# Performance work log

Measured on AMD Instinct MI355X. Metric: run time of the kernel, lower is better.

Reference implementation:

```python
import jax, jax.numpy as jnp
import numpy as np

B, N, I = 8, 1024, 64
E, H, D = 2, 2, 128   # edge types, heads per layer, hidden dim
O = 64                # num_outputs
IN1 = E * H * D       # layer-1 filter input dim (concat of layer-0 heads)


def setup_inputs() -> dict:
    key = jax.random.key(0)
    ks = jax.random.split(key, 20)
    s = lambda f: 1.0 / np.sqrt(f)
    inp = {
        "nodes": jax.random.normal(ks[0], (B, N, I), jnp.float32),
        "edges": jax.random.normal(ks[1], (B, N, N, E), jnp.float32) * 0.1,
        "Wemb": jax.random.normal(ks[2], (I, D), jnp.float32) * s(I),
        "bemb": jnp.zeros((D,), jnp.float32),
        # layer 0 params: filter W, att nets a1/a2 (weight + bias), state bias
        "W0":   jax.random.normal(ks[3], (E, H, D, D), jnp.float32) * s(D),
        "A1w0": jax.random.normal(ks[4], (E, H, D), jnp.float32) * s(D),
        "A1b0": jnp.zeros((E, H), jnp.float32),
        "A2w0": jax.random.normal(ks[5], (E, H, D), jnp.float32) * s(D),
        "A2b0": jnp.zeros((E, H), jnp.float32),
        "SB0":  jnp.zeros((E, H, D), jnp.float32),
        # layer 1 params (input dim = E*H*D from concat)
        "W1":   jax.random.normal(ks[6], (E, H, IN1, D), jnp.float32) * s(IN1),
        "A1w1": jax.random.normal(ks[7], (E, H, D), jnp.float32) * s(D),
        "A1b1": jnp.zeros((E, H), jnp.float32),
        "A2w1": jax.random.normal(ks[8], (E, H, D), jnp.float32) * s(D),
        "A2b1": jnp.zeros((E, H), jnp.float32),
        "SB1":  jnp.zeros((E, H, D), jnp.float32),
        "Wout": jax.random.normal(ks[9], (D, O), jnp.float32) * s(D),
        "bout": jnp.zeros((O,), jnp.float32),
    }
    return inp


def _gat_layer(state, edges_ebnn, W, a1w, a1b, a2w, a2b, sb):
    # state: (B,N,Fin); W: (E,H,Fin,D); edges_ebnn: (E,1,B,N,N)
    Wh = jnp.einsum('bni,ehid->ehbnd', state, W)                    # (E,H,B,N,D)
    s1 = jnp.einsum('ehbnd,ehd->ehbn', Wh, a1w) + a1b[:, :, None, None]
    s2 = jnp.einsum('ehbnd,ehd->ehbn', Wh, a2w) + a2b[:, :, None, None]
    att = s1[..., :, None] + s2[..., None, :]                       # a1_i + a2_j
    att = jax.nn.leaky_relu(att, 0.2) + edges_ebnn                  # edge-type bias
    att = jax.nn.softmax(att, axis=-2)                              # torch dim=1 (over i)
    msg = jnp.einsum('ehbij,ehbjd->ehbid', att, Wh)                 # bmm aggregation
    return msg + sb[:, :, None, None, :]                            # (E,H,B,N,D)


def reference(nodes, edges, Wemb, bemb,
              W0, A1w0, A1b0, A2w0, A2b0, SB0,
              W1, A1w1, A1b1, A2w1, A2b1, SB1,
              Wout, bout):
    edges_e = jnp.transpose(edges, (3, 0, 1, 2))[:, None]           # (E,1,B,N,N)
    state = jax.nn.relu(nodes @ Wemb + bemb)                        # SlimFC embedding
    # layer 0: concat heads/edgetypes along feature dim (torch order jj outer, ii inner)
    m0 = _gat_layer(state, edges_e, W0, A1w0, A1b0, A2w0, A2b0, SB0)
    state = jnp.transpose(m0, (2, 3, 0, 1, 4)).reshape(B, N, E * H * D)
    # layer 1 (last): elu then mean over all heads/edgetypes
    m1 = jax.nn.elu(_gat_layer(state, edges_e, W1, A1w1, A1b1, A2w1, A2b1, SB1))
    state = jnp.mean(m1, axis=(0, 1))                               # (B,N,D)
    return state @ Wout + bout                                      # (B,N,O)
```

## Files before the change

### kernel.cpp

```cpp
#include <hip/hip_runtime.h>
#include <hip/hip_bf16.h>
#include <math.h>

#define NB 8
#define NN 1024
#define NI 64
#define EHC 4
#define ND 128
#define NO 64
#define FIN1 512
#define BN 8192

typedef __attribute__((ext_vector_type(8))) short short8;
typedef __attribute__((ext_vector_type(4))) float f32x4;

__device__ __forceinline__ unsigned short f2bf(float f) {
    union { float f; unsigned u; } v; v.f = f;
    unsigned r = v.u + 0x7FFF + ((v.u >> 16) & 1);
    return (unsigned short)(r >> 16);
}

__global__ void prepTk(const float* __restrict__ W0, const float* __restrict__ W1,
                       const float* __restrict__ Wemb, unsigned short* __restrict__ W0T,
                       unsigned short* __restrict__ W1T, unsigned short* __restrict__ WembT) {
    int idx = blockIdx.x * 256 + threadIdx.x;
    if (idx < EHC * ND * ND) {
        int eh = idx >> 14, d = (idx >> 7) & 127, k = idx & 127;
        W0T[idx] = f2bf(W0[((size_t)(eh * ND + k)) * ND + d]);
    }
    int idx1 = idx - EHC * ND * ND;
    if (idx1 >= 0 && idx1 < EHC * ND * FIN1) {
        int eh = idx1 >> 16;
        int r = idx1 & 65535;
        int d = r >> 9, k = r & 511;
        W1T[idx1] = f2bf(W1[((size_t)(eh * FIN1 + k)) * ND + d]);
    }
    int idx2 = idx - (EHC * ND * ND + EHC * ND * FIN1);
    if (idx2 >= 0 && idx2 < ND * NI) {
        int d = idx2 >> 6, k = idx2 & 63;
        WembT[idx2] = f2bf(Wemb[k * ND + d]);
    }
}

__global__ __launch_bounds__(256, 4) void embwh0k(
    const float* __restrict__ nodes, const unsigned short* __restrict__ WembT,
    const float* __restrict__ bemb, const unsigned short* __restrict__ W0T,
    unsigned short* __restrict__ WhT, const float* __restrict__ a1w,
    const float* __restrict__ a1b, const float* __restrict__ a2w,
    const float* __restrict__ a2b, float* __restrict__ s1, float* __restrict__ s2) {
    int id = blockIdx.x;
    int g = id & 7, s_ = id >> 3;
    int eh = s_ & 3;
    int row0 = ((s_ >> 2) * 8 + g) * 32;
    int t = threadIdx.x;
    int w = t >> 6, lane = t & 63;
    int m = lane & 15, quad = lane >> 4;

    __shared__ unsigned short stateL[32 * 136];

    f32x4 accE[2][2];
#pragma unroll
    for (int mt = 0; mt < 2; ++mt)
#pragma unroll
        for (int nt = 0; nt < 2; ++nt) accE[mt][nt] = (f32x4){0.f, 0.f, 0.f, 0.f};
#pragma unroll
    for (int kt = 0; kt < 2; ++kt) {
        short8 aE[2], bE[2];
#pragma unroll
        for (int mt = 0; mt < 2; ++mt) {
            const float* np = nodes + (size_t)(row0 + mt * 16 + m) * NI + kt * 32 + quad * 8;
            f32x4 v0 = *(const f32x4*)np;
            f32x4 v1 = *(const f32x4*)(np + 4);
            union { unsigned short us[8]; short8 s8; } pk;
#pragma unroll
            for (int r = 0; r < 4; ++r) {
                pk.us[r] = f2bf(v0[r]);
                pk.us[r + 4] = f2bf(v1[r]);
            }
            aE[mt] = pk.s8;
        }
#pragma unroll
        for (int nt = 0; nt < 2; ++nt)
            bE[nt] = *(const short8*)(WembT + (w * 32 + nt * 16 + m) * NI + kt * 32 + quad * 8);
#pragma unroll
        for (int mt = 0; mt < 2; ++mt)
#pragma unroll
            for (int nt = 0; nt < 2; ++nt)
                accE[mt][nt] =
                    __builtin_amdgcn_mfma_f32_16x16x32_bf16(aE[mt], bE[nt], accE[mt][nt], 0, 0, 0);
    }
#pragma unroll
    for (int mt = 0; mt < 2; ++mt)
#pragma unroll
        for (int nt = 0; nt < 2; ++nt) {
            int d = w * 32 + nt * 16 + m;
            float bb = bemb[d];
#pragma unroll
            for (int r = 0; r < 4; ++r) {
                float v = fmaxf(accE[mt][nt][r] + bb, 0.f);
                stateL[(mt * 16 + quad * 4 + r) * 136 + d] = f2bf(v);
            }
        }
    __syncthreads();

    f32x4 acc[2][2];
#pragma unroll
    for (int mt = 0; mt < 2; ++mt)
#pragma unroll
        for (int nt = 0; nt < 2; ++nt) acc[mt][nt] = (f32x4){0.f, 0.f, 0.f, 0.f};
#pragma unroll
    for (int k0 = 0; k0 < ND; k0 += 32) {
        short8 a[2], b[2];
#pragma unroll
        for (int mt = 0; mt < 2; ++mt)
            a[mt] = *(const short8*)&stateL[(mt * 16 + m) * 136 + k0 + quad * 8];
#pragma unroll
        for (int nt = 0; nt < 2; ++nt)
            b[nt] = *(const short8*)(W0T + ((size_t)(eh * ND + w * 32 + nt * 16 + m)) * ND +
                                     k0 + quad * 8);
#pragma unroll
        for (int mt = 0; mt < 2; ++mt)
#pragma unroll
            for (int nt = 0; nt < 2; ++nt)
                acc[mt][nt] =
                    __builtin_amdgcn_mfma_f32_16x16x32_bf16(a[mt], b[nt], acc[mt][nt], 0, 0, 0);
    }

    int b_ = row0 >> 10, i0b = row0 & 1023;
    int ehb = eh * NB + b_;
#pragma unroll
    for (int mt = 0; mt < 2; ++mt)
#pragma unroll
        for (int nt = 0; nt < 2; ++nt) {
            int d = w * 32 + nt * 16 + m;
            int i = i0b + mt * 16 + quad * 4;
            union { unsigned short us[4]; unsigned long long u64; } pk;
#pragma unroll
            for (int r = 0; r < 4; ++r) pk.us[r] = f2bf(acc[mt][nt][r]);
            *(unsigned long long*)(WhT + (((size_t)ehb) * ND + d) * NN + i) = pk.u64;
        }
    float w1a = a1w[eh * ND + w * 32 + m], w1b = a1w[eh * ND + w * 32 + 16 + m];
    float w2a = a2w[eh * ND + w * 32 + m], w2b = a2w[eh * ND + w * 32 + 16 + m];
    float p1[2][4], p2[2][4];
#pragma unroll
    for (int mt = 0; mt < 2; ++mt)
#pragma unroll
        for (int r = 0; r < 4; ++r) {
            p1[mt][r] = acc[mt][0][r] * w1a + acc[mt][1][r] * w1b;
            p2[mt][r] = acc[mt][0][r] * w2a + acc[mt][1][r] * w2b;
        }
#pragma unroll
    for (int off = 8; off >= 1; off >>= 1)
#pragma unroll
        for (int mt = 0; mt < 2; ++mt)
#pragma unroll
            for (int r = 0; r < 4; ++r) {
                p1[mt][r] += __shfl_xor(p1[mt][r], off);
                p2[mt][r] += __shfl_xor(p2[mt][r], off);
            }
    __shared__ float sred[2][4][4][8];
    if (m == 0) {
#pragma unroll
        for (int mt = 0; mt < 2; ++mt)
#pragma unroll
            for (int r = 0; r < 4; ++r) {
                sred[0][w][quad][mt * 4 + r] = p1[mt][r];
                sred[1][w][quad][mt * 4 + r] = p2[mt][r];
            }
    }
    __syncthreads();
    if (t < 32) {
        int mt = t >> 4, quad2 = (t >> 2) & 3, r = t & 3;
        int c = mt * 4 + r;
        float v = sred[0][0][quad2][c] + sred[0][1][quad2][c] + sred[0][2][quad2][c] +
                  sred[0][3][quad2][c];
        s1[(size_t)ehb * NN + i0b + t] = v + a1b[eh];
    } else if (t < 64) {
        int tl = t - 32;
        int mt = tl >> 4, quad2 = (tl >> 2) & 3, r = tl & 3;
        int c = mt * 4 + r;
        float v = sred[1][0][quad2][c] + sred[1][1][quad2][c] + sred[1][2][quad2][c] +
                  sred[1][3][quad2][c];
        s2[(size_t)ehb * NN + i0b + tl] = v + a2b[eh];
    }
}

__global__ __launch_bounds__(256, 4) void whgemm1k(
    const unsigned short* __restrict__ state, const unsigned short* __restrict__ WT,
    unsigned short* __restrict__ WhT, const float* __restrict__ a1w,
    const float* __restrict__ a1b, const float* __restrict__ a2w,
    const float* __restrict__ a2b, float* __restrict__ s1, float* __restrict__ s2) {
    int id = blockIdx.x;
    int g = id & 7, s_ = id >> 3;
    int eh = s_ & 3;
    int row0 = ((s_ >> 2) * 8 + g) * 32;
    int t = threadIdx.x;
    int w = t >> 6, lane = t & 63;
    int m = lane & 15, quad = lane >> 4;

    f32x4 acc[2][2];
#pragma unroll
    for (int mt = 0; mt < 2; ++mt)
#pragma unroll
        for (int nt = 0; nt < 2; ++nt) acc[mt][nt] = (f32x4){0.f, 0.f, 0.f, 0.f};

    const unsigned short* Ab = state + (size_t)(row0 + m) * FIN1 + quad * 8;
    const unsigned short* Bb = WT + ((size_t)eh * ND + w * 32 + m) * FIN1 + quad * 8;
#pragma unroll 4
    for (int k0 = 0; k0 < FIN1; k0 += 32) {
        short8 a[2], b[2];
#pragma unroll
        for (int mt = 0; mt < 2; ++mt)
            a[mt] = *(const short8*)(Ab + (size_t)mt * 16 * FIN1 + k0);
#pragma unroll
        for (int nt = 0; nt < 2; ++nt)
            b[nt] = *(const short8*)(Bb + (size_t)nt * 16 * FIN1 + k0);
#pragma unroll
        for (int mt = 0; mt < 2; ++mt)
#pragma unroll
            for (int nt = 0; nt < 2; ++nt)
                acc[mt][nt] =
                    __builtin_amdgcn_mfma_f32_16x16x32_bf16(a[mt], b[nt], acc[mt][nt], 0, 0, 0);
    }
    int b_ = row0 >> 10, i0b = row0 & 1023;
    int ehb = eh * NB + b_;
#pragma unroll
    for (int mt = 0; mt < 2; ++mt)
#pragma unroll
        for (int nt = 0; nt < 2; ++nt) {
            int d = w * 32 + nt * 16 + m;
            int i = i0b + mt * 16 + quad * 4;
            union { unsigned short us[4]; unsigned long long u64; } pk;
#pragma unroll
            for (int r = 0; r < 4; ++r) pk.us[r] = f2bf(acc[mt][nt][r]);
            *(unsigned long long*)(WhT + (((size_t)ehb) * ND + d) * NN + i) = pk.u64;
        }
    float w1a = a1w[eh * ND + w * 32 + m], w1b = a1w[eh * ND + w * 32 + 16 + m];
    float w2a = a2w[eh * ND + w * 32 + m], w2b = a2w[eh * ND + w * 32 + 16 + m];
    float p1[2][4], p2[2][4];
#pragma unroll
    for (int mt = 0; mt < 2; ++mt)
#pragma unroll
        for (int r = 0; r < 4; ++r) {
            p1[mt][r] = acc[mt][0][r] * w1a + acc[mt][1][r] * w1b;
            p2[mt][r] = acc[mt][0][r] * w2a + acc[mt][1][r] * w2b;
        }
#pragma unroll
    for (int off = 8; off >= 1; off >>= 1)
#pragma unroll
        for (int mt = 0; mt < 2; ++mt)
#pragma unroll
            for (int r = 0; r < 4; ++r) {
                p1[mt][r] += __shfl_xor(p1[mt][r], off);
                p2[mt][r] += __shfl_xor(p2[mt][r], off);
            }
    __shared__ float sred[2][4][4][8];
    if (m == 0) {
#pragma unroll
        for (int mt = 0; mt < 2; ++mt)
#pragma unroll
            for (int r = 0; r < 4; ++r) {
                sred[0][w][quad][mt * 4 + r] = p1[mt][r];
                sred[1][w][quad][mt * 4 + r] = p2[mt][r];
            }
    }
    __syncthreads();
    if (t < 32) {
        int mt = t >> 4, quad2 = (t >> 2) & 3, r = t & 3;
        int c = mt * 4 + r;
        float v = sred[0][0][quad2][c] + sred[0][1][quad2][c] + sred[0][2][quad2][c] +
                  sred[0][3][quad2][c];
        s1[(size_t)ehb * NN + i0b + t] = v + a1b[eh];
    } else if (t < 64) {
        int tl = t - 32;
        int mt = tl >> 4, quad2 = (tl >> 2) & 3, r = tl & 3;
        int c = mt * 4 + r;
        float v = sred[1][0][quad2][c] + sred[1][1][quad2][c] + sred[1][2][quad2][c] +
                  sred[1][3][quad2][c];
        s2[(size_t)ehb * NN + i0b + tl] = v + a2b[eh];
    }
}

__global__ __launch_bounds__(256, 4) void colsumk(const float* __restrict__ edges,
                                                  const float* __restrict__ s1,
                                                  const float* __restrict__ s2,
                                                  float* __restrict__ Spart) {
    int jt = blockIdx.x, b = blockIdx.y, ic = blockIdx.z;
    int t = threadIdx.x;
    int jl = t & 63, is = t >> 6;
    int j = jt * 64 + jl;
    __shared__ float s1L[4][128];
    for (int idx = t; idx < 512; idx += 256) {
        int eh = idx >> 7;
        s1L[eh][idx & 127] = s1[((size_t)eh * NB + b) * NN + ic * 128 + (idx & 127)];
    }
    __syncthreads();
    float s2v[4], acc4[4];
#pragma unroll
    for (int eh = 0; eh < 4; ++eh) {
        s2v[eh] = s2[((size_t)eh * NB + b) * NN + j];
        acc4[eh] = 0.f;
    }
    const float2* ep = (const float2*)edges + ((size_t)(b * NN + ic * 128 + is * 32)) * NN + j;
#pragma unroll 8
    for (int ii = 0; ii < 32; ++ii) {
        float2 ev = ep[(size_t)ii * NN];
        int il = is * 32 + ii;
#pragma unroll
        for (int eh = 0; eh < 4; ++eh) {
            float x = s1L[eh][il] + s2v[eh];
            x = x >= 0.f ? x : 0.2f * x;
            float a = x + (eh < 2 ? ev.x : ev.y);
            acc4[eh] += __expf(a);
        }
    }
    __shared__ float red[4][4][64];
#pragma unroll
    for (int eh = 0; eh < 4; ++eh) red[is][eh][jl] = acc4[eh];
    __syncthreads();
    if (t < 256) {
        int eho = t >> 6, jlo = t & 63;
        float Sv = red[0][eho][jlo] + red[1][eho][jlo] + red[2][eho][jlo] + red[3][eho][jlo];
        Spart[(((size_t)ic * EHC + eho) * NB + b) * NN + jt * 64 + jlo] = Sv;
    }
}

__global__ __launch_bounds__(256, 4) void msgk(const float* __restrict__ edges,
                                               const unsigned short* __restrict__ WhT,
                                               const float* __restrict__ s1,
                                               const float* __restrict__ s2,
                                               const float* __restrict__ Spart,
                                               const float* __restrict__ sb,
                                               unsigned short* __restrict__ out0,
                                               float* __restrict__ out1, int mode) {
    int id = blockIdx.x;
    int b = id & 7;
    int s_ = id >> 3;
    int eh = s_ & 3;
    int itile = s_ >> 2;
    int e = eh >> 1;
    int i0 = itile * 64;
    int t = threadIdx.x;
    int w = t >> 6, lane = t & 63;
    int n = lane & 15, quad = lane >> 4;
    int jl = t & 63, ib = w;

    __shared__ float2 stL[NN];
    __shared__ unsigned short pA[2][64 * 72];

    int base = (eh * NB + b) * NN;
    const size_t pstr = (size_t)EHC * NB * NN;
    for (int jj = t; jj < NN; jj += 256) {
        float S = 0.f;
#pragma unroll
        for (int ic = 0; ic < 8; ++ic) S += Spart[(size_t)ic * pstr + base + jj];
        stL[jj] = make_float2(s2[base + jj], __logf(S));
    }
    float s1r[16];
    {
        const f32x4* sp = (const f32x4*)(s1 + base + i0 + ib * 16);
#pragma unroll
        for (int q4 = 0; q4 < 4; ++q4) {
            f32x4 v = sp[q4];
#pragma unroll
            for (int r = 0; r < 4; ++r) s1r[q4 * 4 + r] = v[r];
        }
    }

    f32x4 acc[2][4];
#pragma unroll
    for (int mt = 0; mt < 2; ++mt)
#pragma unroll
        for (int nt = 0; nt < 4; ++nt) acc[mt][nt] = (f32x4){0.f, 0.f, 0.f, 0.f};

    const unsigned short* Ab =
        WhT + ((size_t)base * ND + (size_t)(w * 32 + n) * NN) + quad * 8;
    const float2* ep = (const float2*)edges + (size_t)(b * NN + i0 + ib * 16) * NN + jl;
    __syncthreads();

    for (int st16 = 0; st16 < 16; ++st16) {
        int j0 = st16 * 64;
        int buf = st16 & 1;
        float2 stj = stL[j0 + jl];
#pragma unroll
        for (int q = 0; q < 16; ++q) {
            float2 ev = ep[(size_t)q * NN + j0];
            float edge = e ? ev.y : ev.x;
            float x = s1r[q] + stj.x;
            x = x >= 0.f ? x : 0.2f * x;
            pA[buf][(ib * 16 + q) * 72 + jl] = f2bf(__expf(x + edge - stj.y));
        }
        __syncthreads();
#pragma unroll
        for (int kt = 0; kt < 2; ++kt) {
            short8 av[2], bv[4];
#pragma unroll
            for (int mt = 0; mt < 2; ++mt)
                av[mt] = *(const short8*)(Ab + (size_t)mt * 16 * NN + kt * 32 + j0);
#pragma unroll
            for (int nt = 0; nt < 4; ++nt)
                bv[nt] = *(const short8*)&pA[buf][(nt * 16 + n) * 72 + kt * 32 + quad * 8];
#pragma unroll
            for (int mt = 0; mt < 2; ++mt)
#pragma unroll
                for (int nt = 0; nt < 4; ++nt)
                    acc[mt][nt] = __builtin_amdgcn_mfma_f32_16x16x32_bf16(av[mt], bv[nt],
                                                                          acc[mt][nt], 0, 0, 0);
        }
    }

#pragma unroll
    for (int mt = 0; mt < 2; ++mt) {
        int d0 = w * 32 + mt * 16 + quad * 4;
        f32x4 sbv = *(const f32x4*)&sb[eh * ND + d0];
#pragma unroll
        for (int nt = 0; nt < 4; ++nt) {
            int i = i0 + nt * 16 + n;
            if (mode == 0) {
                union { unsigned short us[4]; unsigned long long u64; } pk;
#pragma unroll
                for (int r = 0; r < 4; ++r) pk.us[r] = f2bf(acc[mt][nt][r] + sbv[r]);
                *(unsigned long long*)(out0 + (size_t)(b * NN + i) * FIN1 + eh * ND + d0) =
                    pk.u64;
            } else {
                f32x4 vv;
#pragma unroll
                for (int r = 0; r < 4; ++r) {
                    float v = acc[mt][nt][r] + sbv[r];
                    vv[r] = v > 0.f ? v : expm1f(v);
                }
                *(f32x4*)(out1 + ((size_t)(eh * NB + b) * NN + i) * ND + d0) = vv;
            }
        }
    }
}

__global__ __launch_bounds__(256) void finalk(const float* __restrict__ m1,
                                              const float* __restrict__ Wout,
                                              const float* __restrict__ bout,
                                              float* __restrict__ out) {
    int row0 = blockIdx.x * 16;
    int t = threadIdx.x;
    __shared__ float sF[16 * ND];
    __shared__ float wL[ND * NO];
    const size_t str = (size_t)BN * ND;
    for (int idx = t; idx < 16 * ND; idx += 256) {
        size_t r = (size_t)row0 * ND + idx;
        sF[idx] = 0.25f * (m1[r] + m1[r + str] + m1[r + 2 * str] + m1[r + 3 * str]);
    }
    for (int idx = t; idx < ND * NO; idx += 256) wL[idx] = Wout[idx];
    __syncthreads();
    int o = t & 63;
    int rr = t >> 6;
    float bo = bout[o];
#pragma unroll
    for (int q = 0; q < 4; ++q) {
        int r = rr * 4 + q;
        float acc = 0.f;
#pragma unroll 4
        for (int d = 0; d < ND; ++d) acc += sF[r * ND + d] * wL[d * NO + o];
        out[(size_t)(row0 + r) * NO + o] = acc + bo;
    }
}

extern "C" void kernel_launch(void* const* d_in, const int* in_sizes, int n_in,
                              void* d_out, int out_size, void* d_ws, size_t ws_size,
                              hipStream_t stream) {
    const float* nodes = (const float*)d_in[0];
    const float* edges = (const float*)d_in[1];
    const float* Wemb = (const float*)d_in[2];
    const float* bemb = (const float*)d_in[3];
    const float* W0 = (const float*)d_in[4];
    const float* A1w0 = (const float*)d_in[5];
    const float* A1b0 = (const float*)d_in[6];
    const float* A2w0 = (const float*)d_in[7];
    const float* A2b0 = (const float*)d_in[8];
    const float* SB0 = (const float*)d_in[9];
    const float* W1 = (const float*)d_in[10];
    const float* A1w1 = (const float*)d_in[11];
    const float* A1b1 = (const float*)d_in[12];
    const float* A2w1 = (const float*)d_in[13];
    const float* A2b1 = (const float*)d_in[14];
    const float* SB1 = (const float*)d_in[15];
    const float* Wout = (const float*)d_in[16];
    const float* bout = (const float*)d_in[17];
    float* out = (float*)d_out;

    char* p = (char*)d_ws;
    auto alloc = [&](size_t bytes) {
        char* r = p;
        p += (bytes + 255) & ~(size_t)255;
        return r;
    };
    unsigned short* W0T = (unsigned short*)alloc((size_t)EHC * ND * ND * 2);
    unsigned short* W1T = (unsigned short*)alloc((size_t)EHC * ND * FIN1 * 2);
    unsigned short* WembT = (unsigned short*)alloc((size_t)ND * NI * 2);
    unsigned short* WhT = (unsigned short*)alloc((size_t)EHC * BN * ND * 2);
    unsigned short* state1 = (unsigned short*)alloc((size_t)BN * FIN1 * 2);
    float* s1b = (float*)alloc((size_t)EHC * BN * 4);
    float* s2b = (float*)alloc((size_t)EHC * BN * 4);
    float* Spart = (float*)alloc((size_t)8 * EHC * BN * 4);
    float* m1 = (float*)alloc((size_t)EHC * BN * ND * 4);

    prepTk<<<1312, 256, 0, stream>>>(W0, W1, Wemb, W0T, W1T, WembT);
    embwh0k<<<1024, 256, 0, stream>>>(nodes, WembT, bemb, W0T, WhT, A1w0, A1b0, A2w0, A2b0,
                                      s1b, s2b);
    colsumk<<<dim3(NN / 64, NB, 8), 256, 0, stream>>>(edges, s1b, s2b, Spart);
    msgk<<<512, 256, 0, stream>>>(edges, WhT, s1b, s2b, Spart, SB0, state1, m1, 0);
    whgemm1k<<<1024, 256, 0, stream>>>(state1, W1T, WhT, A1w1, A1b1, A2w1, A2b1, s1b, s2b);
    colsumk<<<dim3(NN / 64, NB, 8), 256, 0, stream>>>(edges, s1b, s2b, Spart);
    msgk<<<512, 256, 0, stream>>>(edges, WhT, s1b, s2b, Spart, SB1, state1, m1, 1);
    finalk<<<BN / 16, 256, 0, stream>>>(m1, Wout, bout, out);
}
```

Before: 285.4 us.

## Double-buffer msg kernel loads with 512-thread blocks and vectorize colsum edge reads

The message kernel now runs 512 threads per block. Each wave owns 16 output rows and computes 8 softmax rows, and the edge values and Wh fragments for the next j-tile are prefetched into registers while the current tile runs (software pipelining). Colsum reads edges as float4, covering two j columns per thread, and reduces over 8 partial slices. The aim is to hide global load latency and raise memory throughput. The cost is more registers per thread and more threads per block, which may limit occupancy under launch_bounds(512,4).

```diff
diff --git a/kernel.cpp b/kernel.cpp
--- a/kernel.cpp
+++ b/kernel.cpp
@@ -287,45 +287,57 @@
                                                   float* __restrict__ Spart) {
     int jt = blockIdx.x, b = blockIdx.y, ic = blockIdx.z;
     int t = threadIdx.x;
-    int jl = t & 63, is = t >> 6;
-    int j = jt * 64 + jl;
+    int jp = t & 31, is = t >> 5;
+    int j = jt * 64 + jp * 2;
     __shared__ float s1L[4][128];
     for (int idx = t; idx < 512; idx += 256) {
         int eh = idx >> 7;
         s1L[eh][idx & 127] = s1[((size_t)eh * NB + b) * NN + ic * 128 + (idx & 127)];
     }
     __syncthreads();
-    float s2v[4], acc4[4];
+    float s2v[4][2], acc4[4][2];
 #pragma unroll
     for (int eh = 0; eh < 4; ++eh) {
-        s2v[eh] = s2[((size_t)eh * NB + b) * NN + j];
-        acc4[eh] = 0.f;
-    }
-    const float2* ep = (const float2*)edges + ((size_t)(b * NN + ic * 128 + is * 32)) * NN + j;
-#pragma unroll 8
-    for (int ii = 0; ii < 32; ++ii) {
-        float2 ev = ep[(size_t)ii * NN];
-        int il = is * 32 + ii;
+        s2v[eh][0] = s2[((size_t)eh * NB + b) * NN + j];
+        s2v[eh][1] = s2[((size_t)eh * NB + b) * NN + j + 1];
+        acc4[eh][0] = 0.f;
+        acc4[eh][1] = 0.f;
+    }
+    const float4* ep = (const float4*)edges +
+                       (size_t)(b * NN + ic * 128 + is * 16) * (NN / 2) + jt * 32 + jp;
+#pragma unroll 4
+    for (int ii = 0; ii < 16; ++ii) {
+        float4 ev = ep[(size_t)ii * (NN / 2)];
+        float s1v = s1L[0][is * 16 + ii];
 #pragma unroll
         for (int eh = 0; eh < 4; ++eh) {
-            float x = s1L[eh][il] + s2v[eh];
-            x = x >= 0.f ? x : 0.2f * x;
-            float a = x + (eh < 2 ? ev.x : ev.y);
-            acc4[eh] += __expf(a);
-        }
-    }
-    __shared__ float red[4][4][64];
-#pragma unroll
-    for (int eh = 0; eh < 4; ++eh) red[is][eh][jl] = acc4[eh];
+            float sv = s1L[eh][is * 16 + ii];
+            float x0 = sv + s2v[eh][0];
+            x0 = fmaxf(x0, 0.2f * x0);
+            acc4[eh][0] += __expf(x0 + (eh < 2 ? ev.x : ev.y));
+            float x1 = sv + s2v[eh][1];
+            x1 = fmaxf(x1, 0.2f * x1);
+            acc4[eh][1] += __expf(x1 + (eh < 2 ? ev.z : ev.w));
+        }
+        (void)s1v;
+    }
+    __shared__ float red[8][4][64];
+#pragma unroll
+    for (int eh = 0; eh < 4; ++eh) {
+        red[is][eh][jp * 2] = acc4[eh][0];
+        red[is][eh][jp * 2 + 1] = acc4[eh][1];
+    }
     __syncthreads();
     if (t < 256) {
         int eho = t >> 6, jlo = t & 63;
-        float Sv = red[0][eho][jlo] + red[1][eho][jlo] + red[2][eho][jlo] + red[3][eho][jlo];
+        float Sv = 0.f;
+#pragma unroll
+        for (int isx = 0; isx < 8; ++isx) Sv += red[isx][eho][jlo];
         Spart[(((size_t)ic * EHC + eho) * NB + b) * NN + jt * 64 + jlo] = Sv;
     }
 }
 
-__global__ __launch_bounds__(256, 4) void msgk(const float* __restrict__ edges,
+__global__ __launch_bounds__(512, 4) void msgk(const float* __restrict__ edges,
                                                const unsigned short* __restrict__ WhT,
                                                const float* __restrict__ s1,
                                                const float* __restrict__ s2,
@@ -350,68 +362,80 @@
 
     int base = (eh * NB + b) * NN;
     const size_t pstr = (size_t)EHC * NB * NN;
-    for (int jj = t; jj < NN; jj += 256) {
+    for (int jj = t; jj < NN; jj += 512) {
         float S = 0.f;
 #pragma unroll
         for (int ic = 0; ic < 8; ++ic) S += Spart[(size_t)ic * pstr + base + jj];
         stL[jj] = make_float2(s2[base + jj], __logf(S));
     }
-    float s1r[16];
+    float s1r[8];
     {
-        const f32x4* sp = (const f32x4*)(s1 + base + i0 + ib * 16);
-#pragma unroll
-        for (int q4 = 0; q4 < 4; ++q4) {
-            f32x4 v = sp[q4];
-#pragma unroll
-            for (int r = 0; r < 4; ++r) s1r[q4 * 4 + r] = v[r];
-        }
-    }
-
-    f32x4 acc[2][4];
-#pragma unroll
-    for (int mt = 0; mt < 2; ++mt)
-#pragma unroll
-        for (int nt = 0; nt < 4; ++nt) acc[mt][nt] = (f32x4){0.f, 0.f, 0.f, 0.f};
+        const f32x4* sp = (const f32x4*)(s1 + base + i0 + ib * 8);
+        f32x4 v0 = sp[0], v1 = sp[1];
+#pragma unroll
+        for (int r = 0; r < 4; ++r) { s1r[r] = v0[r]; s1r[r + 4] = v1[r]; }
+    }
+
+    f32x4 acc[4];
+#pragma unroll
+    for (int nt = 0; nt < 4; ++nt) acc[nt] = (f32x4){0.f, 0.f, 0.f, 0.f};
 
     const unsigned short* Ab =
-        WhT + ((size_t)base * ND + (size_t)(w * 32 + n) * NN) + quad * 8;
-    const float2* ep = (const float2*)edges + (size_t)(b * NN + i0 + ib * 16) * NN + jl;
-    __syncthreads();
-
-    for (int st16 = 0; st16 < 16; ++st16) {
-        int j0 = st16 * 64;
-        int buf = st16 & 1;
+        WhT + ((size_t)base * ND + (size_t)(w * 16 + n) * NN) + quad * 8;
+    const float2* ep = (const float2*)edges + (size_t)(b * NN + i0 + ib * 8) * NN + jl;
+    __syncthreads();
+
+    float2 evA[8], evB[8];
+    short8 aA[2], aB[2];
+
+    auto loadE = [&](float2* ev, int j0) {
+#pragma unroll
+        for (int q = 0; q < 8; ++q) ev[q] = ep[(size_t)q * NN + j0];
+    };
+    auto loadA = [&](short8* av, int j0) {
+#pragma unroll
+        for (int kt = 0; kt < 2; ++kt)
+            av[kt] = *(const short8*)(Ab + kt * 32 + j0);
+    };
+    auto pstep = [&](const float2* ev, const short8* av, int j0, int buf) {
         float2 stj = stL[j0 + jl];
 #pragma unroll
-        for (int q = 0; q < 16; ++q) {
-            float2 ev = ep[(size_t)q * NN + j0];
-            float edge = e ? ev.y : ev.x;
+        for (int q = 0; q < 8; ++q) {
+            float edge = e ? ev[q].y : ev[q].x;
             float x = s1r[q] + stj.x;
-            x = x >= 0.f ? x : 0.2f * x;
-            pA[buf][(ib * 16 + q) * 72 + jl] = f2bf(__expf(x + edge - stj.y));
+            x = fmaxf(x, 0.2f * x);
+            pA[buf][(ib * 8 + q) * 72 + jl] = f2bf(__expf(x + edge - stj.y));
         }
         __syncthreads();
 #pragma unroll
         for (int kt = 0; kt < 2; ++kt) {
-            short8 av[2], bv[4];
-#pragma unroll
-            for (int mt = 0; mt < 2; ++mt)
-                av[mt] = *(const short8*)(Ab + (size_t)mt * 16 * NN + kt * 32 + j0);
+            short8 bv[4];
 #pragma unroll
             for (int nt = 0; nt < 4; ++nt)
                 bv[nt] = *(const short8*)&pA[buf][(nt * 16 + n) * 72 + kt * 32 + quad * 8];
 #pragma unroll
-            for (int mt = 0; mt < 2; ++mt)
-#pragma unroll
-                for (int nt = 0; nt < 4; ++nt)
-                    acc[mt][nt] = __builtin_amdgcn_mfma_f32_16x16x32_bf16(av[mt], bv[nt],
-                                                                          acc[mt][nt], 0, 0, 0);
-        }
-    }
-
-#pragma unroll
-    for (int mt = 0; mt < 2; ++mt) {
-        int d0 = w * 32 + mt * 16 + quad * 4;
+            for (int nt = 0; nt < 4; ++nt)
+                acc[nt] =
+                    __builtin_amdgcn_mfma_f32_16x16x32_bf16(av[kt], bv[nt], acc[nt], 0, 0, 0);
+        }
+    };
+
+    loadE(evA, 0);
+    loadA(aA, 0);
+    for (int sp2 = 0; sp2 < 8; ++sp2) {
+        int j0 = sp2 * 128;
+        loadE(evB, j0 + 64);
+        loadA(aB, j0 + 64);
+        pstep(evA, aA, j0, 0);
+        if (sp2 < 7) {
+            loadE(evA, j0 + 128);
+            loadA(aA, j0 + 128);
+        }
+        pstep(evB, aB, j0 + 64, 1);
+    }
+
+    {
+        int d0 = w * 16 + quad * 4;
         f32x4 sbv = *(const f32x4*)&sb[eh * ND + d0];
 #pragma unroll
         for (int nt = 0; nt < 4; ++nt) {
@@ -419,14 +443,14 @@
             if (mode == 0) {
                 union { unsigned short us[4]; unsigned long long u64; } pk;
 #pragma unroll
-                for (int r = 0; r < 4; ++r) pk.us[r] = f2bf(acc[mt][nt][r] + sbv[r]);
+                for (int r = 0; r < 4; ++r) pk.us[r] = f2bf(acc[nt][r] + sbv[r]);
                 *(unsigned long long*)(out0 + (size_t)(b * NN + i) * FIN1 + eh * ND + d0) =
                     pk.u64;
             } else {
                 f32x4 vv;
 #pragma unroll
                 for (int r = 0; r < 4; ++r) {
-                    float v = acc[mt][nt][r] + sbv[r];
+                    float v = acc[nt][r] + sbv[r];
                     vv[r] = v > 0.f ? v : expm1f(v);
                 }
                 *(f32x4*)(out1 + ((size_t)(eh * NB + b) * NN + i) * ND + d0) = vv;
@@ -506,9 +530,9 @@
     embwh0k<<<1024, 256, 0, stream>>>(nodes, WembT, bemb, W0T, WhT, A1w0, A1b0, A2w0, A2b0,
                                       s1b, s2b);
     colsumk<<<dim3(NN / 64, NB, 8), 256, 0, stream>>>(edges, s1b, s2b, Spart);
-    msgk<<<512, 256, 0, stream>>>(edges, WhT, s1b, s2b, Spart, SB0, state1, m1, 0);
+    msgk<<<512, 512, 0, stream>>>(edges, WhT, s1b, s2b, Spart, SB0, state1, m1, 0);
     whgemm1k<<<1024, 256, 0, stream>>>(state1, W1T, WhT, A1w1, A1b1, A2w1, A2b1, s1b, s2b);
     colsumk<<<dim3(NN / 64, NB, 8), 256, 0, stream>>>(edges, s1b, s2b, Spart);
-    msgk<<<512, 256, 0, stream>>>(edges, WhT, s1b, s2b, Spart, SB1, state1, m1, 1);
+    msgk<<<512, 512, 0, stream>>>(edges, WhT, s1b, s2b, Spart, SB1, state1, m1, 1);
     finalk<<<BN / 16, 256, 0, stream>>>(m1, Wout, bout, out);
 }
```

Measured after the change: 274.2 us. 1.04x faster.
